# Performance work log

Measured on AMD Instinct MI355X. Metric: run time of the kernel, lower is better.

Reference implementation:

```python
import jax, jax.numpy as jnp
import numpy as np

CHW = (1, 256, 256)
NPH, NPW = 16, 16
NB = 8          # n_blocks
D = 384         # hidden_d
H = 6           # n_heads
DH = D // H     # d_head = 64
OUT = 4
PH, PW = CHW[1] // NPH, CHW[2] // NPW
IN_D = CHW[0] * PH * PW        # 256
S = NPH * NPW + 1              # 257 tokens (CLS + patches)
EPS = 1e-5                     # torch LayerNorm default


def positional_embeddings(seq_len, d):
    # matches get_positional_embeddings: sin(i/10000^(j/d)) even j, cos(i/10000^((j-1)/d)) odd j
    i = jnp.arange(seq_len, dtype=jnp.float32)[:, None]
    j = jnp.arange(d, dtype=jnp.float32)[None, :]
    j_eff = jnp.where(j % 2 == 0, j, j - 1)
    ang = i / jnp.power(jnp.float32(10000.0), j_eff / d)
    return jnp.where(j % 2 == 0, jnp.sin(ang), jnp.cos(ang))


def patchify(images):
    # (n,c,h,w) -> (n, NPH*NPW, c*PH*PW), patch flattened channel-first like patch.flatten()
    n, c, h, w = images.shape
    x = images.reshape(n, c, NPH, PH, NPW, PW)
    x = x.transpose(0, 2, 4, 1, 3, 5)  # n, nph, npw, c, ph, pw
    return x.reshape(n, NPH * NPW, c * PH * PW)


def layernorm(x, g, b):
    mu = jnp.mean(x, axis=-1, keepdims=True)
    var = jnp.mean(jnp.square(x - mu), axis=-1, keepdims=True)
    return (x - mu) * jax.lax.rsqrt(var + EPS) * g + b


def mhsa(x, Wq, bq, Wk, bk, Wv, bv):
    # x: [B,S,D]; W*: [H,DH,DH] (torch Linear convention out=x@W.T+b), b*: [H,DH]
    B = x.shape[0]
    xh = x.reshape(B, S, H, DH)
    q = jnp.einsum('bshd,hed->bshe', xh, Wq) + bq
    k = jnp.einsum('bshd,hed->bshe', xh, Wk) + bk
    v = jnp.einsum('bshd,hed->bshe', xh, Wv) + bv
    scores = jnp.einsum('bqhe,bkhe->bhqk', q, k) / jnp.float32(DH) ** 0.5
    attn = jax.nn.softmax(scores, axis=-1)
    o = jnp.einsum('bhqk,bkhe->bqhe', attn, v)
    return o.reshape(B, S, D)


def setup_inputs() -> dict:
    key = jax.random.key(0)
    ks = jax.random.split(key, 24)
    s = 0.02
    B = 64
    inp = {
        'images': jax.random.normal(ks[0], (B, *CHW), jnp.float32),
        'Wmap': jax.random.normal(ks[1], (D, IN_D), jnp.float32) * s,
        'bmap': jax.random.normal(ks[2], (D,), jnp.float32) * s,
        'cls': jax.random.uniform(ks[3], (1, D), jnp.float32),
        'ln1_g': jnp.ones((NB, D), jnp.float32),
        'ln1_b': jnp.zeros((NB, D), jnp.float32),
        'Wq': jax.random.normal(ks[4], (NB, H, DH, DH), jnp.float32) * s,
        'bq': jax.random.normal(ks[5], (NB, H, DH), jnp.float32) * s,
        'Wk': jax.random.normal(ks[6], (NB, H, DH, DH), jnp.float32) * s,
        'bk': jax.random.normal(ks[7], (NB, H, DH), jnp.float32) * s,
        'Wv': jax.random.normal(ks[8], (NB, H, DH, DH), jnp.float32) * s,
        'bv': jax.random.normal(ks[9], (NB, H, DH), jnp.float32) * s,
        'ln2_g': jnp.ones((NB, D), jnp.float32),
        'ln2_b': jnp.zeros((NB, D), jnp.float32),
        'W1': jax.random.normal(ks[10], (NB, 4 * D, D), jnp.float32) * s,
        'b1': jax.random.normal(ks[11], (NB, 4 * D), jnp.float32) * s,
        'W2': jax.random.normal(ks[12], (NB, D, 4 * D), jnp.float32) * s,
        'b2': jax.random.normal(ks[13], (NB, D), jnp.float32) * s,
        'Wout': jax.random.normal(ks[14], (OUT, D), jnp.float32) * s,
        'bout': jax.random.normal(ks[15], (OUT,), jnp.float32) * s,
    }
    return inp


def reference(images, Wmap, bmap, cls, ln1_g, ln1_b, Wq, bq, Wk, bk, Wv, bv,
              ln2_g, ln2_b, W1, b1, W2, b2, Wout, bout):
    B = images.shape[0]
    patches = patchify(images)                        # [B, S-1, IN_D]
    tokens = patches @ Wmap.T + bmap                  # [B, S-1, D]
    tokens = jnp.concatenate([jnp.broadcast_to(cls[None], (B, 1, D)), tokens], axis=1)
    out = tokens + positional_embeddings(S, D)[None]  # [B, S, D]
    for blk in range(NB):
        out = out + mhsa(layernorm(out, ln1_g[blk], ln1_b[blk]),
                         Wq[blk], bq[blk], Wk[blk], bk[blk], Wv[blk], bv[blk])
        h = layernorm(out, ln2_g[blk], ln2_b[blk])
        h = jax.nn.gelu(h @ W1[blk].T + b1[blk], approximate=False)
        out = out + (h @ W2[blk].T + b2[blk])
    cls_out = out[:, 0]                               # [B, D]
    return jax.nn.softmax(cls_out @ Wout.T + bout, axis=-1)
```

## Files before the change

kernel.cpp:

```cpp
#include <hip/hip_runtime.h>

typedef __bf16 bf16x8 __attribute__((ext_vector_type(8)));
typedef float f32x4 __attribute__((ext_vector_type(4)));
typedef unsigned short u16;
typedef unsigned short u16x4 __attribute__((ext_vector_type(4)));

typedef __attribute__((address_space(3))) unsigned int as3_u32;
typedef __attribute__((address_space(1))) unsigned int as1_u32;

static __device__ __forceinline__ float b2f(u16 u) {
    union { unsigned int ui; float f; } v; v.ui = ((unsigned int)u) << 16; return v.f;
}
static __device__ __forceinline__ u16 f2b(float f) {
    union { float f; unsigned int u; } v; v.f = f;
    unsigned int r = v.u + 0x7FFFu + ((v.u >> 16) & 1u);
    return (u16)(r >> 16);
}
static __device__ __forceinline__ float pos_emb(int s, int d) {
    int je = d & ~1;
    float ang = (float)s * powf(10000.0f, -(float)je / 384.0f);
    return (d & 1) ? cosf(ang) : sinf(ang);
}
static __device__ __forceinline__ float gelu_f(float t) {
    return 0.5f * t * (1.0f + erff(t * 0.70710678118654752f));
}
static __device__ __forceinline__ void async16(const void* g, void* l) {
    __builtin_amdgcn_global_load_lds((const as1_u32*)g, (as3_u32*)l, 16, 0, 0);
}

#define MFMA16 __builtin_amdgcn_mfma_f32_16x16x32_bf16

static __device__ __forceinline__ void mm32(const u16* __restrict__ A, int lda,
                                            const u16* __restrict__ B, int ldb,
                                            int K, f32x4 acc[2][2], int lane) {
    const int r  = lane & 15;
    const int kr = (lane >> 4) << 3;
    const u16* pa0 = A + (size_t)r * lda + kr;
    const u16* pa1 = pa0 + (size_t)16 * lda;
    const u16* pb0 = B + (size_t)r * ldb + kr;
    const u16* pb1 = pb0 + (size_t)16 * ldb;
    for (int k0 = 0; k0 < K; k0 += 32) {
        bf16x8 a0 = *(const bf16x8*)(pa0 + k0);
        bf16x8 a1 = *(const bf16x8*)(pa1 + k0);
        bf16x8 b0 = *(const bf16x8*)(pb0 + k0);
        bf16x8 b1 = *(const bf16x8*)(pb1 + k0);
        acc[0][0] = MFMA16(a0, b0, acc[0][0], 0, 0, 0);
        acc[0][1] = MFMA16(a0, b1, acc[0][1], 0, 0, 0);
        acc[1][0] = MFMA16(a1, b0, acc[1][0], 0, 0, 0);
        acc[1][1] = MFMA16(a1, b1, acc[1][1], 0, 0, 0);
    }
}

template<int K>
static __device__ __forceinline__ void stage_tile(const u16* __restrict__ gbase,
                                                  u16* lds, int kt, int t) {
#pragma unroll
    for (int j = 0; j < 4; j++) {
        int o = j * 4096 + t * 16;
        int row = o >> 7;
        int c = (o >> 4) & 7;
        int gc = c ^ (row & 7);
        const u16* src = gbase + (size_t)row * K + kt * 64 + gc * 8;
        async16(src, (char*)lds + o);
    }
}

template<int K, int EPI>
__global__ __launch_bounds__(256) void k_gemm128(const u16* __restrict__ A,
                                                 const u16* __restrict__ Bw,
                                                 const float* __restrict__ bias,
                                                 u16* __restrict__ out16,
                                                 float* __restrict__ xres,
                                                 int m0g) {
    __shared__ u16 lds[2][2][128 * 64];
    const int t = threadIdx.x;
    const int NY = gridDim.y;
    int nwg = gridDim.x * NY;
    int flat = blockIdx.x + gridDim.x * blockIdx.y;
    int q8 = nwg >> 3, r8 = nwg & 7, xcd = flat & 7, idx = flat >> 3;
    int wg = (xcd < r8 ? xcd * (q8 + 1) : r8 * (q8 + 1) + (xcd - r8) * q8) + idx;
    const int mt = wg / NY, nt = wg - mt * NY;

    const u16* Ab = A + (size_t)mt * 128 * K;
    const u16* Bb = Bw + (size_t)nt * 128 * K;
    constexpr int NKT = K / 64;
    const int lane = t & 63, w = t >> 6;
    const int wm = (w >> 1) * 64, wn = (w & 1) * 64;
    const int r = lane & 15, g = lane >> 4;

    stage_tile<K>(Ab, lds[0][0], 0, t);
    stage_tile<K>(Bb, lds[0][1], 0, t);

    f32x4 acc[4][4] = {};
    for (int kt = 0; kt < NKT; kt++) {
        if (kt + 1 < NKT) {
            stage_tile<K>(Ab, lds[(kt + 1) & 1][0], kt + 1, t);
            stage_tile<K>(Bb, lds[(kt + 1) & 1][1], kt + 1, t);
            asm volatile("s_waitcnt vmcnt(8)" ::: "memory");
        } else {
            asm volatile("s_waitcnt vmcnt(0)" ::: "memory");
        }
        __builtin_amdgcn_sched_barrier(0);
        __builtin_amdgcn_s_barrier();
        __builtin_amdgcn_sched_barrier(0);
        const u16* ldsA = lds[kt & 1][0];
        const u16* ldsB = lds[kt & 1][1];
#pragma unroll
        for (int ks = 0; ks < 2; ks++) {
            bf16x8 a[4], b[4];
#pragma unroll
            for (int i = 0; i < 4; i++) {
                int ra = wm + i * 16 + r;
                int ca = (ks * 4 + g) ^ (ra & 7);
                a[i] = *(const bf16x8*)((const char*)ldsA + ra * 128 + ca * 16);
                int rb = wn + i * 16 + r;
                int cb = (ks * 4 + g) ^ (rb & 7);
                b[i] = *(const bf16x8*)((const char*)ldsB + rb * 128 + cb * 16);
            }
            __builtin_amdgcn_s_setprio(1);
#pragma unroll
            for (int i = 0; i < 4; i++)
#pragma unroll
                for (int jj = 0; jj < 4; jj++)
                    acc[i][jj] = MFMA16(a[i], b[jj], acc[i][jj], 0, 0, 0);
            __builtin_amdgcn_s_setprio(0);
        }
        __builtin_amdgcn_s_barrier();
    }
#pragma unroll
    for (int i = 0; i < 4; i++) {
#pragma unroll
        for (int q = 0; q < 4; q++) {
            int ml = mt * 128 + wm + i * 16 + g * 4 + q;
#pragma unroll
            for (int jj = 0; jj < 4; jj++) {
                int n = nt * 128 + wn + jj * 16 + r;
                float v = acc[i][jj][q] + bias[n];
                if (EPI == 0) {
                    out16[(size_t)ml * 1536 + n] = f2b(gelu_f(v));
                } else {
                    int m = m0g + ml;
                    if (m < 16448) xres[(size_t)m * 384 + n] += v;
                }
            }
        }
    }
}

__global__ __launch_bounds__(64) void k_fattn(const u16* __restrict__ qb,
                                              const u16* __restrict__ kb,
                                              const u16* __restrict__ vT,
                                              float* __restrict__ x) {
    __shared__ u16 pl[32][40];
    const int lane = threadIdx.x;
    int flat = blockIdx.x;
    int xcd = flat & 7, idx = flat >> 3;
    int lbh = idx / 9;
    const int bh = xcd * 48 + lbh;
    const int q0 = (idx - lbh * 9) * 32;
    const int b = bh / 6, h = bh - b * 6;
    const int r = lane & 15, g = lane >> 4;

    const u16* qbase = qb + ((size_t)b * 257) * 384 + h * 64;
    const u16* kbase = kb + ((size_t)b * 257) * 384 + h * 64;
    const u16* vbase = vT + ((size_t)bh * 64) * 288;

    bf16x8 qf[2][2];
#pragma unroll
    for (int ti = 0; ti < 2; ti++)
#pragma unroll
        for (int kh = 0; kh < 2; kh++)
            qf[ti][kh] = *(const bf16x8*)(qbase + (size_t)(q0 + ti * 16 + r) * 384 + kh * 32 + g * 8);

    f32x4 accO[2][2][2] = {};
    f32x4 sum_[2] = {};

    for (int kv0 = 0; kv0 < 288; kv0 += 32) {
        bf16x8 kf[2][2];
#pragma unroll
        for (int tj = 0; tj < 2; tj++)
#pragma unroll
            for (int kh = 0; kh < 2; kh++)
                kf[tj][kh] = *(const bf16x8*)(kbase + (size_t)(kv0 + tj * 16 + r) * 384 + kh * 32 + g * 8);
        bf16x8 vf[2][2];
#pragma unroll
        for (int eT = 0; eT < 2; eT++)
#pragma unroll
            for (int tjE = 0; tjE < 2; tjE++)
                vf[eT][tjE] = *(const bf16x8*)(vbase + (size_t)(eT * 32 + tjE * 16 + r) * 288 + kv0 + g * 8);

        f32x4 s_[2][2] = {};
#pragma unroll
        for (int ti = 0; ti < 2; ti++)
#pragma unroll
            for (int tj = 0; tj < 2; tj++) {
                s_[ti][tj] = MFMA16(qf[ti][0], kf[tj][0], s_[ti][tj], 0, 0, 0);
                s_[ti][tj] = MFMA16(qf[ti][1], kf[tj][1], s_[ti][tj], 0, 0, 0);
            }
#pragma unroll
        for (int ti = 0; ti < 2; ti++) {
#pragma unroll
            for (int tj = 0; tj < 2; tj++) {
                bool bad = (kv0 + tj * 16 + r) >= 257;
#pragma unroll
                for (int q = 0; q < 4; q++) {
                    float p = bad ? 0.f : __expf(s_[ti][tj][q] * 0.125f);
                    s_[ti][tj][q] = p;
                }
                sum_[ti] += s_[ti][tj];
#pragma unroll
                for (int q = 0; q < 4; q++)
                    pl[ti * 16 + g * 4 + q][tj * 16 + r] = f2b(s_[ti][tj][q]);
            }
        }
        bf16x8 pa[2];
#pragma unroll
        for (int ti2 = 0; ti2 < 2; ti2++)
            pa[ti2] = *(const bf16x8*)&pl[ti2 * 16 + r][g * 8];
#pragma unroll
        for (int eT = 0; eT < 2; eT++)
#pragma unroll
            for (int ti2 = 0; ti2 < 2; ti2++)
#pragma unroll
                for (int tjE = 0; tjE < 2; tjE++)
                    accO[eT][ti2][tjE] = MFMA16(pa[ti2], vf[eT][tjE], accO[eT][ti2][tjE], 0, 0, 0);
    }
#pragma unroll
    for (int o = 1; o < 16; o <<= 1)
#pragma unroll
        for (int ti = 0; ti < 2; ti++)
#pragma unroll
            for (int q = 0; q < 4; q++)
                sum_[ti][q] += __shfl_xor(sum_[ti][q], o, 64);
#pragma unroll
    for (int ti = 0; ti < 2; ti++)
#pragma unroll
        for (int q = 0; q < 4; q++) {
            int qi = q0 + ti * 16 + g * 4 + q;
            if (qi < 257) {
                float inv = 1.0f / sum_[ti][q];
                float* px = x + ((size_t)b * 257 + qi) * 384 + h * 64;
#pragma unroll
                for (int eT = 0; eT < 2; eT++)
#pragma unroll
                    for (int tjE = 0; tjE < 2; tjE++)
                        px[eT * 32 + tjE * 16 + r] += accO[eT][ti][tjE][q] * inv;
            }
        }
}

__global__ __launch_bounds__(256) void k_cvt16(const void* __restrict__ src, u16* __restrict__ dst,
                                               int n, const unsigned* __restrict__ probe) {
    const bool isf32 = (*probe == 0x3F800000u);
    int i0 = (blockIdx.x * 256 + threadIdx.x) * 4;
    if (isf32) {
        const float* s = (const float*)src;
#pragma unroll
        for (int j = 0; j < 4; j++) { int i = i0 + j; if (i < n) dst[i] = f2b(s[i]); }
    } else {
        const u16* s = (const u16*)src;
#pragma unroll
        for (int j = 0; j < 4; j++) { int i = i0 + j; if (i < n) dst[i] = s[i]; }
    }
}
__global__ __launch_bounds__(256) void k_cvt32(const void* __restrict__ src, float* __restrict__ dst,
                                               int n, const unsigned* __restrict__ probe) {
    const bool isf32 = (*probe == 0x3F800000u);
    int i0 = (blockIdx.x * 256 + threadIdx.x) * 4;
    if (isf32) {
        const float* s = (const float*)src;
#pragma unroll
        for (int j = 0; j < 4; j++) { int i = i0 + j; if (i < n) dst[i] = s[i]; }
    } else {
        const u16* s = (const u16*)src;
#pragma unroll
        for (int j = 0; j < 4; j++) { int i = i0 + j; if (i < n) dst[i] = b2f(s[i]); }
    }
}

__global__ __launch_bounds__(256) void k_vtpad(u16* __restrict__ vT) {
    int idx = blockIdx.x * 256 + threadIdx.x;
    const int total = 384 * 64 * 31;
    if (idx < total) {
        int be = idx / 31; int s = 257 + (idx - be * 31);
        vT[(size_t)be * 288 + s] = 0;
    }
}

__global__ __launch_bounds__(256) void k_patch(const u16* __restrict__ img,
                                               const u16* __restrict__ Wmap,
                                               const float* __restrict__ bmap,
                                               float* __restrict__ x) {
    const int lane = threadIdx.x & 63;
    const int wv = threadIdx.x >> 6;
    const int mt = blockIdx.x * 4 + wv;
    const int nt = blockIdx.y;
    const int m0 = mt * 32, n0 = nt * 32;
    const int r = lane & 15, kr = (lane >> 4) << 3;
    f32x4 acc[2][2] = {};
    int ma = m0 + r;
    size_t base0 = (size_t)(ma >> 8) * 65536 + (size_t)((ma >> 4) & 15) * 4096 + (size_t)(ma & 15) * 16;
    ma += 16;
    size_t base1 = (size_t)(ma >> 8) * 65536 + (size_t)((ma >> 4) & 15) * 4096 + (size_t)(ma & 15) * 16;
    const u16* pb0 = Wmap + (size_t)(n0 + r) * 256 + kr;
    const u16* pb1 = pb0 + 16 * 256;
    for (int k0 = 0; k0 < 256; k0 += 32) {
        int k = k0 + kr;
        size_t off = (size_t)(k >> 4) * 256 + (k & 15);
        bf16x8 a0 = *(const bf16x8*)(img + base0 + off);
        bf16x8 a1 = *(const bf16x8*)(img + base1 + off);
        bf16x8 b0 = *(const bf16x8*)(pb0 + k0);
        bf16x8 b1 = *(const bf16x8*)(pb1 + k0);
        acc[0][0] = MFMA16(a0, b0, acc[0][0], 0, 0, 0);
        acc[0][1] = MFMA16(a0, b1, acc[0][1], 0, 0, 0);
        acc[1][0] = MFMA16(a1, b0, acc[1][0], 0, 0, 0);
        acc[1][1] = MFMA16(a1, b1, acc[1][1], 0, 0, 0);
    }
#pragma unroll
    for (int ti = 0; ti < 2; ti++)
#pragma unroll
        for (int i = 0; i < 4; i++) {
            int m = m0 + ti * 16 + ((lane >> 4) << 2) + i;
            int b = m >> 8, p = m & 255, s = p + 1;
            float* px = x + ((size_t)b * 257 + s) * 384;
#pragma unroll
            for (int tj = 0; tj < 2; tj++) {
                int n = n0 + tj * 16 + (lane & 15);
                px[n] = acc[ti][tj][i] + bmap[n] + pos_emb(s, n);
            }
        }
}

__global__ __launch_bounds__(384) void k_cls(const float* __restrict__ cls, float* __restrict__ x) {
    int b = blockIdx.x, d = threadIdx.x;
    x[(size_t)b * 257 * 384 + d] = cls[d] + pos_emb(0, d);
}

__global__ __launch_bounds__(256) void k_ln(const float* __restrict__ x,
                                            const float* __restrict__ g,
                                            const float* __restrict__ bb,
                                            u16* __restrict__ xn) {
    const int lane = threadIdx.x & 63, wv = threadIdx.x >> 6;
    const int row = blockIdx.x * 16 + wv * 4 + (lane >> 4);
    const int r = lane & 15;
    const float* px = x + (size_t)row * 384;
    f32x4 v[6]; float s = 0.f;
#pragma unroll
    for (int i = 0; i < 6; i++) {
        v[i] = *(const f32x4*)(px + i * 64 + r * 4);
        s += v[i][0] + v[i][1] + v[i][2] + v[i][3];
    }
#pragma unroll
    for (int o = 1; o < 16; o <<= 1) s += __shfl_xor(s, o, 64);
    float mu = s * (1.0f / 384.0f);
    float q = 0.f;
#pragma unroll
    for (int i = 0; i < 6; i++)
#pragma unroll
        for (int j = 0; j < 4; j++) { float d = v[i][j] - mu; q += d * d; }
#pragma unroll
    for (int o = 1; o < 16; o <<= 1) q += __shfl_xor(q, o, 64);
    float rstd = rsqrtf(q * (1.0f / 384.0f) + 1e-5f);
    u16* po = xn + (size_t)row * 384;
#pragma unroll
    for (int i = 0; i < 6; i++) {
        int d0 = i * 64 + r * 4;
        f32x4 gg = *(const f32x4*)(g + d0);
        f32x4 bv = *(const f32x4*)(bb + d0);
        u16x4 o4;
#pragma unroll
        for (int j = 0; j < 4; j++) o4[j] = f2b((v[i][j] - mu) * rstd * gg[j] + bv[j]);
        *(u16x4*)(po + d0) = o4;
    }
}

__global__ __launch_bounds__(256) void k_qkv3(const u16* __restrict__ xn,
                                              const u16* __restrict__ Wq,
                                              const u16* __restrict__ Wk,
                                              const u16* __restrict__ Wv,
                                              const float* __restrict__ bq,
                                              const float* __restrict__ bk,
                                              const float* __restrict__ bv,
                                              u16* __restrict__ qo,
                                              u16* __restrict__ ko,
                                              u16* __restrict__ vT) {
    const int lane = threadIdx.x & 63, wv = threadIdx.x >> 6;
    int nwg = 129 * 36;
    int flat = blockIdx.x + 129 * blockIdx.y;
    int q8 = nwg >> 3, r8 = nwg & 7, xcd = flat & 7, idx = flat >> 3;
    int wg = (xcd < r8 ? xcd * (q8 + 1) : r8 * (q8 + 1) + (xcd - r8) * q8) + idx;
    int bxx = wg / 36, yy = wg - bxx * 36;

    const int mt = bxx * 4 + wv; if (mt >= 514) return;
    const int ty = yy / 12, rest = yy - ty * 12;
    const int nt = rest & 1, h = rest >> 1;
    const u16* W = (ty == 0) ? Wq : (ty == 1) ? Wk : Wv;
    const float* bias = (ty == 0) ? bq : (ty == 1) ? bk : bv;
    f32x4 acc[2][2] = {};
    mm32(xn + (size_t)(mt * 32) * 384 + h * 64, 384,
         W + ((size_t)h * 64 + nt * 32) * 64, 64, 64, acc, lane);
#pragma unroll
    for (int ti = 0; ti < 2; ti++)
#pragma unroll
        for (int i = 0; i < 4; i++) {
            int m = mt * 32 + ti * 16 + ((lane >> 4) << 2) + i;
#pragma unroll
            for (int tj = 0; tj < 2; tj++) {
                int nl = nt * 32 + tj * 16 + (lane & 15);
                float v = acc[ti][tj][i] + bias[h * 64 + nl];
                if (ty == 0) {
                    qo[(size_t)m * 384 + h * 64 + nl] = f2b(v);
                } else if (ty == 1) {
                    ko[(size_t)m * 384 + h * 64 + nl] = f2b(v);
                } else {
                    int b = m / 257, s = m - b * 257;
                    vT[(((size_t)b * 6 + h) * 64 + nl) * 288 + s] = f2b(v);
                }
            }
        }
}

__global__ __launch_bounds__(256) void k_head(const float* __restrict__ x,
                                              const float* __restrict__ Wout,
                                              const float* __restrict__ bout,
                                              float* __restrict__ out) {
    int t = threadIdx.x; int b = t >> 2, o = t & 3;
    const float* px = x + (size_t)b * 257 * 384;
    const float* pw = Wout + o * 384;
    float s = 0.f;
    for (int d = 0; d < 384; d++) s += px[d] * pw[d];
    s += bout[o];
    float mx = fmaxf(s, __shfl_xor(s, 1, 4));
    mx = fmaxf(mx, __shfl_xor(mx, 2, 4));
    float e = expf(s - mx);
    float sm = e + __shfl_xor(e, 1, 4);
    sm += __shfl_xor(sm, 2, 4);
    out[t] = e / sm;
}

extern "C" void kernel_launch(void* const* d_in, const int* in_sizes, int n_in,
                              void* d_out, int out_size, void* d_ws, size_t ws_size,
                              hipStream_t stream) {
    const unsigned* probe = (const unsigned*)d_in[4];

    char* w = (char*)d_ws;
    size_t used = 0;
    auto alloc = [&](size_t bytes) -> char* {
        char* p = w + used; used += (bytes + 255) & ~(size_t)255; return p;
    };
    float* x   = (float*)alloc(16448ull * 384 * 4);
    u16*   xn  = (u16*)  alloc(16512ull * 384 * 2);
    u16*   qb  = (u16*)  alloc((16448ull + 32) * 384 * 2);
    u16*   kb  = (u16*)  alloc((16448ull + 32) * 384 * 2);
    u16*   vT  = (u16*)  alloc(384ull * 64 * 288 * 2);
    u16*   imB = (u16*)  alloc(4194304ull * 2);
    u16*   WmB = (u16*)  alloc(98304ull * 2);
    u16*   WqB = (u16*)  alloc(196608ull * 2);
    u16*   WkB = (u16*)  alloc(196608ull * 2);
    u16*   WvB = (u16*)  alloc(196608ull * 2);
    u16*   W1B = (u16*)  alloc(4718592ull * 2);
    u16*   W2B = (u16*)  alloc(4718592ull * 2);
    float* prm = (float*)alloc(39172ull * 4);
    char*  flexp = w + used;
    size_t flex = (ws_size > used) ? (ws_size - used) : 0;

    long long ft = (long long)(flex / (128ull * 1536 * 2));
    int FT128 = (ft > 129) ? 129 : (int)ft;
    if (FT128 < 1) FT128 = 1;
    u16* hb = (u16*)flexp;

    float* bmapF = prm + 0;
    float* clsF  = prm + 384;
    float* ln1gF = prm + 768;
    float* ln1bF = prm + 3840;
    float* bqF   = prm + 6912;
    float* bkF   = prm + 9984;
    float* bvF   = prm + 13056;
    float* ln2gF = prm + 16128;
    float* ln2bF = prm + 19200;
    float* b1F   = prm + 22272;
    float* b2F   = prm + 34560;
    float* WoutF = prm + 37632;
    float* boutF = prm + 39168;

    dim3 B256(256);
    auto cvt16 = [&](const void* src, u16* dst, int n) {
        hipLaunchKernelGGL(k_cvt16, dim3((n + 1023) / 1024), B256, 0, stream, src, dst, n, probe);
    };
    auto cvt32 = [&](const void* src, float* dst, int n) {
        hipLaunchKernelGGL(k_cvt32, dim3((n + 1023) / 1024), B256, 0, stream, src, dst, n, probe);
    };
    cvt16(d_in[0],  imB, 4194304);
    cvt16(d_in[1],  WmB, 98304);
    cvt16(d_in[6],  WqB, 196608);
    cvt16(d_in[8],  WkB, 196608);
    cvt16(d_in[10], WvB, 196608);
    cvt16(d_in[14], W1B, 4718592);
    cvt16(d_in[16], W2B, 4718592);
    cvt32(d_in[2],  bmapF, 384);
    cvt32(d_in[3],  clsF,  384);
    cvt32(d_in[4],  ln1gF, 3072);
    cvt32(d_in[5],  ln1bF, 3072);
    cvt32(d_in[7],  bqF,   3072);
    cvt32(d_in[9],  bkF,   3072);
    cvt32(d_in[11], bvF,   3072);
    cvt32(d_in[12], ln2gF, 3072);
    cvt32(d_in[13], ln2bF, 3072);
    cvt32(d_in[15], b1F,   12288);
    cvt32(d_in[17], b2F,   3072);
    cvt32(d_in[18], WoutF, 1536);
    cvt32(d_in[19], boutF, 4);
    (void)in_sizes; (void)n_in; (void)out_size;

    hipMemsetAsync(xn + 16448ull * 384, 0, 64ull * 384 * 2, stream);

    hipLaunchKernelGGL(k_vtpad, dim3((384 * 64 * 31 + 255) / 256), B256, 0, stream, vT);
    hipLaunchKernelGGL(k_patch, dim3(128, 12), B256, 0, stream, imB, WmB, bmapF, x);
    hipLaunchKernelGGL(k_cls, dim3(64), dim3(384), 0, stream, clsF, x);
    for (int blk = 0; blk < 8; blk++) {
        hipLaunchKernelGGL(k_ln, dim3(1028), B256, 0, stream, x, ln1gF + blk * 384, ln1bF + blk * 384, xn);
        hipLaunchKernelGGL(k_qkv3, dim3(129, 36), B256, 0, stream, xn,
                           WqB + (size_t)blk * 24576, WkB + (size_t)blk * 24576, WvB + (size_t)blk * 24576,
                           bqF + blk * 384, bkF + blk * 384, bvF + blk * 384,
                           qb, kb, vT);
        hipLaunchKernelGGL(k_fattn, dim3(3456), dim3(64), 0, stream, qb, kb, vT, x);
        hipLaunchKernelGGL(k_ln, dim3(1028), B256, 0, stream, x, ln2gF + blk * 384, ln2bF + blk * 384, xn);
        for (int T0 = 0; T0 < 129; T0 += FT128) {
            int nt = (129 - T0 < FT128) ? (129 - T0) : FT128;
            k_gemm128<384, 0><<<dim3(nt, 12), B256, 0, stream>>>(
                xn + (size_t)T0 * 128 * 384, W1B + (size_t)blk * 1536 * 384,
                b1F + blk * 1536, hb, nullptr, 0);
            k_gemm128<1536, 1><<<dim3(nt, 3), B256, 0, stream>>>(
                hb, W2B + (size_t)blk * 384 * 1536,
                b2F + blk * 384, nullptr, x, T0 * 128);
        }
    }
    hipLaunchKernelGGL(k_head, dim3(1), B256, 0, stream, x, WoutF, boutF, (float*)d_out);
}
```

Baseline: 1.469 ms.

## Fuse Q/K/V projections per block, single-buffer GEMM LDS, fast erf GELU

The QKV kernel now loads each activation tile once and computes all three Q, K and V projections from it, shrinking the grid from 36 to 12 column groups so xn is read a third as often. The 128-tile GEMM drops its double-buffered LDS prefetch and instead loads each K-tile and waits on it before computing. This halves shared memory and may raise occupancy, but it removes the overlap of loads with MFMA work. GELU's erff is replaced by the Abramowitz–Stegun polynomial with a hardware reciprocal and __expf, which is cheaper but only approximate (about 1e-7 absolute error).

```diff
diff --git a/kernel.cpp b/kernel.cpp
--- a/kernel.cpp
+++ b/kernel.cpp
@@ -21,35 +21,22 @@
     float ang = (float)s * powf(10000.0f, -(float)je / 384.0f);
     return (d & 1) ? cosf(ang) : sinf(ang);
 }
-static __device__ __forceinline__ float gelu_f(float t) {
-    return 0.5f * t * (1.0f + erff(t * 0.70710678118654752f));
+static __device__ __forceinline__ float gelu_f(float x) {
+    float xs = x * 0.70710678118654752f;
+    float ax = fabsf(xs);
+    float t = __builtin_amdgcn_rcpf(1.0f + 0.3275911f * ax);
+    float poly = ((((1.061405429f * t - 1.453152027f) * t + 1.421413741f) * t
+                   - 0.284496736f) * t + 0.254829592f) * t;
+    float e = __expf(-ax * ax);
+    float erfv = 1.0f - poly * e;
+    erfv = (xs < 0.f) ? -erfv : erfv;
+    return 0.5f * x * (1.0f + erfv);
 }
 static __device__ __forceinline__ void async16(const void* g, void* l) {
     __builtin_amdgcn_global_load_lds((const as1_u32*)g, (as3_u32*)l, 16, 0, 0);
 }
 
 #define MFMA16 __builtin_amdgcn_mfma_f32_16x16x32_bf16
-
-static __device__ __forceinline__ void mm32(const u16* __restrict__ A, int lda,
-                                            const u16* __restrict__ B, int ldb,
-                                            int K, f32x4 acc[2][2], int lane) {
-    const int r  = lane & 15;
-    const int kr = (lane >> 4) << 3;
-    const u16* pa0 = A + (size_t)r * lda + kr;
-    const u16* pa1 = pa0 + (size_t)16 * lda;
-    const u16* pb0 = B + (size_t)r * ldb + kr;
-    const u16* pb1 = pb0 + (size_t)16 * ldb;
-    for (int k0 = 0; k0 < K; k0 += 32) {
-        bf16x8 a0 = *(const bf16x8*)(pa0 + k0);
-        bf16x8 a1 = *(const bf16x8*)(pa1 + k0);
-        bf16x8 b0 = *(const bf16x8*)(pb0 + k0);
-        bf16x8 b1 = *(const bf16x8*)(pb1 + k0);
-        acc[0][0] = MFMA16(a0, b0, acc[0][0], 0, 0, 0);
-        acc[0][1] = MFMA16(a0, b1, acc[0][1], 0, 0, 0);
-        acc[1][0] = MFMA16(a1, b0, acc[1][0], 0, 0, 0);
-        acc[1][1] = MFMA16(a1, b1, acc[1][1], 0, 0, 0);
-    }
-}
 
 template<int K>
 static __device__ __forceinline__ void stage_tile(const u16* __restrict__ gbase,
@@ -72,7 +59,7 @@
                                                  u16* __restrict__ out16,
                                                  float* __restrict__ xres,
                                                  int m0g) {
-    __shared__ u16 lds[2][2][128 * 64];
+    __shared__ u16 lds[2][128 * 64];
     const int t = threadIdx.x;
     const int NY = gridDim.y;
     int nwg = gridDim.x * NY;
@@ -88,23 +75,14 @@
     const int wm = (w >> 1) * 64, wn = (w & 1) * 64;
     const int r = lane & 15, g = lane >> 4;
 
-    stage_tile<K>(Ab, lds[0][0], 0, t);
-    stage_tile<K>(Bb, lds[0][1], 0, t);
-
     f32x4 acc[4][4] = {};
     for (int kt = 0; kt < NKT; kt++) {
-        if (kt + 1 < NKT) {
-            stage_tile<K>(Ab, lds[(kt + 1) & 1][0], kt + 1, t);
-            stage_tile<K>(Bb, lds[(kt + 1) & 1][1], kt + 1, t);
-            asm volatile("s_waitcnt vmcnt(8)" ::: "memory");
-        } else {
-            asm volatile("s_waitcnt vmcnt(0)" ::: "memory");
-        }
+        stage_tile<K>(Ab, lds[0], kt, t);
+        stage_tile<K>(Bb, lds[1], kt, t);
+        asm volatile("s_waitcnt vmcnt(0)" ::: "memory");
         __builtin_amdgcn_sched_barrier(0);
         __builtin_amdgcn_s_barrier();
         __builtin_amdgcn_sched_barrier(0);
-        const u16* ldsA = lds[kt & 1][0];
-        const u16* ldsB = lds[kt & 1][1];
 #pragma unroll
         for (int ks = 0; ks < 2; ks++) {
             bf16x8 a[4], b[4];
@@ -112,10 +90,10 @@
             for (int i = 0; i < 4; i++) {
                 int ra = wm + i * 16 + r;
                 int ca = (ks * 4 + g) ^ (ra & 7);
-                a[i] = *(const bf16x8*)((const char*)ldsA + ra * 128 + ca * 16);
+                a[i] = *(const bf16x8*)((const char*)lds[0] + ra * 128 + ca * 16);
                 int rb = wn + i * 16 + r;
                 int cb = (ks * 4 + g) ^ (rb & 7);
-                b[i] = *(const bf16x8*)((const char*)ldsB + rb * 128 + cb * 16);
+                b[i] = *(const bf16x8*)((const char*)lds[1] + rb * 128 + cb * 16);
             }
             __builtin_amdgcn_s_setprio(1);
 #pragma unroll
@@ -385,39 +363,61 @@
                                               u16* __restrict__ ko,
                                               u16* __restrict__ vT) {
     const int lane = threadIdx.x & 63, wv = threadIdx.x >> 6;
-    int nwg = 129 * 36;
+    int nwg = 129 * 12;
     int flat = blockIdx.x + 129 * blockIdx.y;
     int q8 = nwg >> 3, r8 = nwg & 7, xcd = flat & 7, idx = flat >> 3;
     int wg = (xcd < r8 ? xcd * (q8 + 1) : r8 * (q8 + 1) + (xcd - r8) * q8) + idx;
-    int bxx = wg / 36, yy = wg - bxx * 36;
+    int bxx = wg / 12, rest = wg - bxx * 12;
 
     const int mt = bxx * 4 + wv; if (mt >= 514) return;
-    const int ty = yy / 12, rest = yy - ty * 12;
     const int nt = rest & 1, h = rest >> 1;
-    const u16* W = (ty == 0) ? Wq : (ty == 1) ? Wk : Wv;
-    const float* bias = (ty == 0) ? bq : (ty == 1) ? bk : bv;
-    f32x4 acc[2][2] = {};
-    mm32(xn + (size_t)(mt * 32) * 384 + h * 64, 384,
-         W + ((size_t)h * 64 + nt * 32) * 64, 64, 64, acc, lane);
-#pragma unroll
-    for (int ti = 0; ti < 2; ti++)
-#pragma unroll
-        for (int i = 0; i < 4; i++) {
-            int m = mt * 32 + ti * 16 + ((lane >> 4) << 2) + i;
-#pragma unroll
-            for (int tj = 0; tj < 2; tj++) {
-                int nl = nt * 32 + tj * 16 + (lane & 15);
-                float v = acc[ti][tj][i] + bias[h * 64 + nl];
-                if (ty == 0) {
-                    qo[(size_t)m * 384 + h * 64 + nl] = f2b(v);
-                } else if (ty == 1) {
-                    ko[(size_t)m * 384 + h * 64 + nl] = f2b(v);
-                } else {
-                    int b = m / 257, s = m - b * 257;
-                    vT[(((size_t)b * 6 + h) * 64 + nl) * 288 + s] = f2b(v);
+    const int r = lane & 15, kr = (lane >> 4) << 3;
+
+    const u16* Abase = xn + (size_t)(mt * 32) * 384 + h * 64;
+    bf16x8 a00 = *(const bf16x8*)(Abase + (size_t)r * 384 + kr);
+    bf16x8 a10 = *(const bf16x8*)(Abase + (size_t)(16 + r) * 384 + kr);
+    bf16x8 a01 = *(const bf16x8*)(Abase + (size_t)r * 384 + 32 + kr);
+    bf16x8 a11 = *(const bf16x8*)(Abase + (size_t)(16 + r) * 384 + 32 + kr);
+
+    const u16* Ws[3] = { Wq, Wk, Wv };
+    const float* bs[3] = { bq, bk, bv };
+#pragma unroll
+    for (int ty = 0; ty < 3; ty++) {
+        const u16* Bb = Ws[ty] + ((size_t)h * 64 + nt * 32) * 64;
+        bf16x8 b00 = *(const bf16x8*)(Bb + (size_t)r * 64 + kr);
+        bf16x8 b10 = *(const bf16x8*)(Bb + (size_t)(16 + r) * 64 + kr);
+        bf16x8 b01 = *(const bf16x8*)(Bb + (size_t)r * 64 + 32 + kr);
+        bf16x8 b11 = *(const bf16x8*)(Bb + (size_t)(16 + r) * 64 + 32 + kr);
+        f32x4 acc[2][2] = {};
+        acc[0][0] = MFMA16(a00, b00, acc[0][0], 0, 0, 0);
+        acc[0][1] = MFMA16(a00, b10, acc[0][1], 0, 0, 0);
+        acc[1][0] = MFMA16(a10, b00, acc[1][0], 0, 0, 0);
+        acc[1][1] = MFMA16(a10, b10, acc[1][1], 0, 0, 0);
+        acc[0][0] = MFMA16(a01, b01, acc[0][0], 0, 0, 0);
+        acc[0][1] = MFMA16(a01, b11, acc[0][1], 0, 0, 0);
+        acc[1][0] = MFMA16(a11, b01, acc[1][0], 0, 0, 0);
+        acc[1][1] = MFMA16(a11, b11, acc[1][1], 0, 0, 0);
+        const float* bias = bs[ty];
+#pragma unroll
+        for (int ti = 0; ti < 2; ti++)
+#pragma unroll
+            for (int i = 0; i < 4; i++) {
+                int m = mt * 32 + ti * 16 + ((lane >> 4) << 2) + i;
+#pragma unroll
+                for (int tj = 0; tj < 2; tj++) {
+                    int nl = nt * 32 + tj * 16 + (lane & 15);
+                    float v = acc[ti][tj][i] + bias[h * 64 + nl];
+                    if (ty == 0) {
+                        qo[(size_t)m * 384 + h * 64 + nl] = f2b(v);
+                    } else if (ty == 1) {
+                        ko[(size_t)m * 384 + h * 64 + nl] = f2b(v);
+                    } else {
+                        int b = m / 257, s = m - b * 257;
+                        vT[(((size_t)b * 6 + h) * 64 + nl) * 288 + s] = f2b(v);
+                    }
                 }
             }
-        }
+    }
 }
 
 __global__ __launch_bounds__(256) void k_head(const float* __restrict__ x,
@@ -519,7 +519,7 @@
     hipLaunchKernelGGL(k_cls, dim3(64), dim3(384), 0, stream, clsF, x);
     for (int blk = 0; blk < 8; blk++) {
         hipLaunchKernelGGL(k_ln, dim3(1028), B256, 0, stream, x, ln1gF + blk * 384, ln1bF + blk * 384, xn);
-        hipLaunchKernelGGL(k_qkv3, dim3(129, 36), B256, 0, stream, xn,
+        hipLaunchKernelGGL(k_qkv3, dim3(129, 12), B256, 0, stream, xn,
                            WqB + (size_t)blk * 24576, WkB + (size_t)blk * 24576, WvB + (size_t)blk * 24576,
                            bqF + blk * 384, bkF + blk * 384, bvF + blk * 384,
                            qb, kb, vT);
```

After: 1.401 ms. -4.6%, faster.
